# Kernel optimization log

Hardware: AMD Instinct MI355X
Metric: run time of the kernel (lower is better)

Reference implementation:

```python
import jax, jax.numpy as jnp
import numpy as np

NUM_HEADS = 8
WINDOW = 128  # num_previous_frames
EPS = 1e-5


def setup_inputs() -> dict:
    key = jax.random.key(0)
    ks = jax.random.split(key, 5)
    B, T, E = 8, 1024, 512
    x = jax.random.normal(ks[0], (B, T, E), dtype=jnp.float32)
    x_lengths = jax.random.randint(ks[1], (B,), 1, T + 1).astype(jnp.int32)
    gamma = jnp.ones((E,), dtype=jnp.float32)
    beta = jnp.zeros((E,), dtype=jnp.float32)
    sc_in = 1.0 / np.sqrt(E)
    w_in = jax.random.normal(ks[2], (3 * E, E), dtype=jnp.float32) * sc_in
    b_in = jnp.zeros((3 * E,), dtype=jnp.float32)
    w_out = jax.random.normal(ks[3], (E, E), dtype=jnp.float32) * sc_in
    b_out = jnp.zeros((E,), dtype=jnp.float32)
    return {"x": x, "x_lengths": x_lengths, "gamma": gamma, "beta": beta,
            "w_in": w_in, "b_in": b_in, "w_out": w_out, "b_out": b_out}


def _forward(x, gamma, beta, w_in, b_in, w_out, b_out):
    B, T, E = x.shape
    H = NUM_HEADS
    D = E // H
    # Timewise LayerNorm: normalize over channel dim per (batch, time)
    mu = jnp.mean(x, axis=-1, keepdims=True)
    var = jnp.mean(jnp.square(x - mu), axis=-1, keepdims=True)
    xn = (x - mu) * jax.lax.rsqrt(var + EPS) * gamma + beta
    # in-projection: qkv packed
    qkv = xn @ w_in.T + b_in  # [B,T,3E]
    q, k, v = jnp.split(qkv, 3, axis=-1)
    q = q.reshape(B, T, H, D)
    k = k.reshape(B, T, H, D)
    v = v.reshape(B, T, H, D)
    scale = 1.0 / np.sqrt(D)
    scores = jnp.einsum('bqhd,bkhd->bhqk', q * scale, k)  # [B,H,T,T]
    # banded causal mask: allow j in [i-WINDOW, i]
    i = jnp.arange(T)[:, None]
    j = jnp.arange(T)[None, :]
    allowed = (j <= i) & (j >= i - WINDOW)
    scores = jnp.where(allowed[None, None], scores, -jnp.inf)
    attn = jax.nn.softmax(scores, axis=-1)
    ctx = jnp.einsum('bhqk,bkhd->bqhd', attn, v).reshape(B, T, E)
    out = ctx @ w_out.T + b_out
    return out  # dropout is identity in eval mode


def reference(x, x_lengths, gamma, beta, w_in, b_in, w_out, b_out):
    del x_lengths  # unused by the original forward (no key_padding_mask passed)
    return _forward(x, gamma, beta, w_in, b_in, w_out, b_out)
```

## Files before the change

kernel.cpp:

```cpp
#include <hip/hip_runtime.h>
#include <stdint.h>

typedef __bf16 bf16;
typedef __bf16 bf16x8 __attribute__((ext_vector_type(8)));
typedef float f32x4 __attribute__((ext_vector_type(4)));

#define MFMA_16x16x32(a, b, c) __builtin_amdgcn_mfma_f32_16x16x32_bf16((a), (b), (c), 0, 0, 0)

__device__ __forceinline__ void gl_lds16(const bf16* g, bf16* l) {
    __builtin_amdgcn_global_load_lds(
        (const __attribute__((address_space(1))) void*)g,
        (__attribute__((address_space(3))) void*)l, 16, 0, 0);
}

__device__ __forceinline__ void prep_unit(int u, const float* __restrict__ x,
                                          const float* __restrict__ gamma,
                                          const float* __restrict__ beta,
                                          const float* __restrict__ w_in,
                                          const float* __restrict__ w_out,
                                          bf16* __restrict__ xn,
                                          bf16* __restrict__ cw_in,
                                          bf16* __restrict__ cw_out) {
    const int tid = threadIdx.x;
    if (u < 2048) {
        const int lane = tid & 63;
        const int row = (u << 2) + (tid >> 6);
        const size_t base = (size_t)row * 512 + lane * 8;
        const float* xf = x + base;
        float4 a = *(const float4*)xf;
        float4 b = *(const float4*)(xf + 4);
        float f[8] = {a.x, a.y, a.z, a.w, b.x, b.y, b.z, b.w};
        float s = 0.f;
#pragma unroll
        for (int j = 0; j < 8; ++j) s += f[j];
#pragma unroll
        for (int off = 32; off >= 1; off >>= 1) s += __shfl_xor(s, off, 64);
        const float mu = s * (1.0f / 512.0f);
        float vs = 0.f;
#pragma unroll
        for (int j = 0; j < 8; ++j) { float d = f[j] - mu; vs += d * d; }
#pragma unroll
        for (int off = 32; off >= 1; off >>= 1) vs += __shfl_xor(vs, off, 64);
        const float rstd = rsqrtf(vs * (1.0f / 512.0f) + 1e-5f);
        float4 g0 = *(const float4*)(gamma + lane * 8);
        float4 g1 = *(const float4*)(gamma + lane * 8 + 4);
        float4 b0 = *(const float4*)(beta + lane * 8);
        float4 b1 = *(const float4*)(beta + lane * 8 + 4);
        float gg[8] = {g0.x, g0.y, g0.z, g0.w, g1.x, g1.y, g1.z, g1.w};
        float bb[8] = {b0.x, b0.y, b0.z, b0.w, b1.x, b1.y, b1.z, b1.w};
        bf16x8 o;
#pragma unroll
        for (int j = 0; j < 8; ++j)
            o[j] = (bf16)((f[j] - mu) * rstd * gg[j] + bb[j]);
        *(bf16x8*)(xn + base) = o;
    } else {
        const float* src;
        bf16* dst;
        int base;
        if (u < 2432) { src = w_in;  dst = cw_in;  base = (u - 2048) * 2048; }
        else          { src = w_out; dst = cw_out; base = (u - 2432) * 2048; }
        const int i = base + tid * 8;
        float4 a = *(const float4*)(src + i);
        float4 b = *(const float4*)(src + i + 4);
        float f[8] = {a.x, a.y, a.z, a.w, b.x, b.y, b.z, b.w};
        bf16x8 o;
#pragma unroll
        for (int j = 0; j < 8; ++j) o[j] = (bf16)f[j];
        *(bf16x8*)(dst + i) = o;
    }
}

template <int TM, int TN, typename OT>
__device__ __forceinline__ void gemm_tile(const bf16* __restrict__ A,
                                          const bf16* __restrict__ B,
                                          const float* __restrict__ bias,
                                          OT* __restrict__ C,
                                          int N, int K, int m0, int n0,
                                          char* smem) {
    constexpr int MI = TM / 32, NI = TN / 32;
    bf16* As = (bf16*)smem;
    bf16* Bs = (bf16*)(smem + TM * 128);
    const int tid = threadIdx.x;
    const int lane = tid & 63;
    const int wid = tid >> 6;
    const int wm = (wid >> 1) * (TM / 2), wn = (wid & 1) * (TN / 2);
    const int l15 = lane & 15, l16 = lane >> 4;

    f32x4 acc[MI][NI] = {};

    const bf16* Abase = A + (size_t)m0 * K;
    const bf16* Bbase = B + (size_t)n0 * K;

    for (int k0 = 0; k0 < K; k0 += 64) {
#pragma unroll
        for (int c = tid; c < TM * 8; c += 256) {
            const int p = c / (TM * 4);
            const int r = (c % (TM * 4)) >> 2;
            const int ko = (c & 3) * 8 + p * 32;
            gl_lds16(Abase + (size_t)r * K + k0 + ko, &As[c * 8]);
        }
#pragma unroll
        for (int c = tid; c < TN * 8; c += 256) {
            const int p = c / (TN * 4);
            const int r = (c % (TN * 4)) >> 2;
            const int ko = (c & 3) * 8 + p * 32;
            gl_lds16(Bbase + (size_t)r * K + k0 + ko, &Bs[c * 8]);
        }
        __syncthreads();
#pragma unroll
        for (int h = 0; h < 2; ++h) {
            bf16x8 af[MI], bfr[NI];
#pragma unroll
            for (int t = 0; t < MI; ++t)
                af[t] = *(const bf16x8*)&As[h * (TM * 32) + (wm + t * 16 + l15) * 32 + l16 * 8];
#pragma unroll
            for (int t = 0; t < NI; ++t)
                bfr[t] = *(const bf16x8*)&Bs[h * (TN * 32) + (wn + t * 16 + l15) * 32 + l16 * 8];
#pragma unroll
            for (int i = 0; i < MI; ++i)
#pragma unroll
                for (int j = 0; j < NI; ++j)
                    acc[i][j] = MFMA_16x16x32(af[i], bfr[j], acc[i][j]);
        }
        __syncthreads();
    }

#pragma unroll
    for (int j = 0; j < NI; ++j) {
        const int col = n0 + wn + j * 16 + l15;
        const float bv = bias[col];
#pragma unroll
        for (int i = 0; i < MI; ++i) {
            const int rbase = m0 + wm + i * 16 + l16 * 4;
#pragma unroll
            for (int r = 0; r < 4; ++r)
                C[(size_t)(rbase + r) * N + col] = (OT)(acc[i][j][r] + bv);
        }
    }
}

#define KS_STRIDE 72
#define VN_STRIDE 74
#define PW_STRIDE 40

__device__ __forceinline__ void attn_unit(int qtile, int bh,
                                          const bf16* __restrict__ qkv,
                                          bf16* __restrict__ ctx,
                                          char* smem) {
    bf16* Ks   = (bf16*)smem;
    bf16* Vn   = (bf16*)(smem + 9216);
    bf16* Pbuf = (bf16*)(smem + 18688);

    const int tid = threadIdx.x;
    const int lane = tid & 63, wid = tid >> 6;
    const int l15 = lane & 15, l16 = lane >> 4;
    const int b = bh >> 3, h = bh & 7;
    const int q0 = qtile * 64;
    const int kv0 = (q0 > 128) ? (q0 - 128) : 0;
    const size_t tokbase = (size_t)b * 1024;

    const int qt0 = q0 + wid * 16;
    const bf16* qptr = qkv + (tokbase + qt0 + l15) * 1536 + h * 64;
    bf16x8 qa0 = *(const bf16x8*)(qptr + l16 * 8);
    bf16x8 qa1 = *(const bf16x8*)(qptr + 32 + l16 * 8);

    bf16* Pw = &Pbuf[wid * 16 * PW_STRIDE];
    f32x4 of[4] = {};
    float mst[4], lst[4];
#pragma unroll
    for (int r = 0; r < 4; ++r) { mst[r] = -1e30f; lst[r] = 0.f; }

    const int ktstart = ((qt0 > 128) ? (qt0 - 128) : 0) & ~31;
    const int ktend = qt0 + 15;

    for (int c0 = kv0; c0 < q0 + 64; c0 += 64) {
        for (int c = tid; c < 512; c += 256) {
            const int kk = c >> 3, dc = (c & 7) * 8;
            const bf16* src = qkv + (tokbase + c0 + kk) * 1536 + h * 64 + dc;
            *(uint4*)&Ks[kk * KS_STRIDE + dc] = *(const uint4*)(src + 512);
            uint4 vw = *(const uint4*)(src + 1024);
            uint* vdst = (uint*)&Vn[kk * VN_STRIDE + dc];
            vdst[0] = vw.x; vdst[1] = vw.y; vdst[2] = vw.z; vdst[3] = vw.w;
        }
        __syncthreads();

        const int klo = (ktstart > c0) ? ktstart : c0;
        const int khi = (ktend < c0 + 63) ? ktend : c0 + 63;
        for (int kt = klo; kt <= khi; kt += 32) {
            const int krel = kt - c0;
            f32x4 s0 = {}, s1 = {};
            {
                const bf16* kb0 = &Ks[(krel + l15) * KS_STRIDE + l16 * 8];
                const bf16* kb1 = kb0 + 16 * KS_STRIDE;
                s0 = MFMA_16x16x32(qa0, *(const bf16x8*)kb0, s0);
                s0 = MFMA_16x16x32(qa1, *(const bf16x8*)(kb0 + 32), s0);
                s1 = MFMA_16x16x32(qa0, *(const bf16x8*)kb1, s1);
                s1 = MFMA_16x16x32(qa1, *(const bf16x8*)(kb1 + 32), s1);
            }
            float e0[4], e1[4];
#pragma unroll
            for (int r = 0; r < 4; ++r) {
                const int qa = qt0 + l16 * 4 + r;
                const int kg0 = kt + l15;
                const int kg1 = kg0 + 16;
                const bool ok0 = (kg0 <= qa) && (kg0 >= qa - 128);
                const bool ok1 = (kg1 <= qa) && (kg1 >= qa - 128);
                float v0 = ok0 ? s0[r] * 0.125f : -1e30f;
                float v1 = ok1 ? s1[r] * 0.125f : -1e30f;
                float mx = fmaxf(v0, v1);
#pragma unroll
                for (int off = 1; off < 16; off <<= 1)
                    mx = fmaxf(mx, __shfl_xor(mx, off, 64));
                const float mnew = fmaxf(mst[r], mx);
                const float alpha = __expf(mst[r] - mnew);
                e0[r] = ok0 ? __expf(v0 - mnew) : 0.f;
                e1[r] = ok1 ? __expf(v1 - mnew) : 0.f;
                float rs = e0[r] + e1[r];
#pragma unroll
                for (int off = 1; off < 16; off <<= 1)
                    rs += __shfl_xor(rs, off, 64);
                lst[r] = lst[r] * alpha + rs;
                mst[r] = mnew;
#pragma unroll
                for (int nt = 0; nt < 4; ++nt) of[nt][r] *= alpha;
            }
#pragma unroll
            for (int r = 0; r < 4; ++r) {
                const int q = l16 * 4 + r;
                Pw[q * PW_STRIDE + l15] = (bf16)e0[r];
                Pw[q * PW_STRIDE + 16 + l15] = (bf16)e1[r];
            }
            __asm__ volatile("s_waitcnt lgkmcnt(0)" ::: "memory");
            bf16x8 pa = *(const bf16x8*)&Pw[l15 * PW_STRIDE + l16 * 8];
#pragma unroll
            for (int nt = 0; nt < 4; ++nt) {
                bf16x8 vb;
#pragma unroll
                for (int j = 0; j < 8; ++j)
                    vb[j] = Vn[(krel + l16 * 8 + j) * VN_STRIDE + nt * 16 + l15];
                of[nt] = MFMA_16x16x32(pa, vb, of[nt]);
            }
            __asm__ volatile("s_waitcnt lgkmcnt(0)" ::: "memory");
        }
        __syncthreads();
    }

    float linv[4];
#pragma unroll
    for (int r = 0; r < 4; ++r) linv[r] = 1.0f / lst[r];
    bf16* cbase = ctx + (tokbase + qt0) * 512 + h * 64;
#pragma unroll
    for (int nt = 0; nt < 4; ++nt)
#pragma unroll
        for (int r = 0; r < 4; ++r) {
            const int q = l16 * 4 + r;
            cbase[(size_t)q * 512 + nt * 16 + l15] = (bf16)(of[nt][r] * linv[r]);
        }
}

__global__ __launch_bounds__(256) void prep_kernel(const float* x, const float* gamma,
                                                   const float* beta, const float* w_in,
                                                   const float* w_out, bf16* xn,
                                                   bf16* cw_in, bf16* cw_out) {
    prep_unit(blockIdx.x, x, gamma, beta, w_in, w_out, xn, cw_in, cw_out);
}

__global__ __launch_bounds__(256) void gemm_qkv_kernel(const bf16* A, const bf16* B,
                                                       const float* bias, bf16* C) {
    __shared__ __align__(16) char smem[32768];
    gemm_tile<128, 128, bf16>(A, B, bias, C, 1536, 512,
                              blockIdx.y * 128, blockIdx.x * 128, smem);
}

__global__ __launch_bounds__(256) void attn_kernel(const bf16* qkv, bf16* ctx) {
    __shared__ __align__(16) char smem[23808];
    attn_unit(blockIdx.x >> 6, blockIdx.x & 63, qkv, ctx, smem);
}

__global__ __launch_bounds__(256) void gemm_out_kernel(const bf16* A, const bf16* B,
                                                       const float* bias, float* C) {
    __shared__ __align__(16) char smem[24576];
    gemm_tile<128, 64, float>(A, B, bias, C, 512, 512,
                              (blockIdx.x >> 3) * 128, (blockIdx.x & 7) * 64, smem);
}

extern "C" void kernel_launch(void* const* d_in, const int* in_sizes, int n_in,
                              void* d_out, int out_size, void* d_ws, size_t ws_size,
                              hipStream_t stream) {
    const float* x     = (const float*)d_in[0];
    const float* gamma = (const float*)d_in[2];
    const float* beta  = (const float*)d_in[3];
    const float* w_in  = (const float*)d_in[4];
    const float* b_in  = (const float*)d_in[5];
    const float* w_out = (const float*)d_in[6];
    const float* b_out = (const float*)d_in[7];
    float* out = (float*)d_out;
    char* ws = (char*)d_ws;

    bf16* cw_in  = (bf16*)ws;
    bf16* cw_out = cw_in + 786432;
    bf16* xn     = (bf16*)(ws + (4u << 20));
    bf16* qkv    = (bf16*)(ws + (12u << 20));
    bf16* ctx    = xn;

    prep_kernel<<<2560, 256, 0, stream>>>(x, gamma, beta, w_in, w_out, xn, cw_in, cw_out);
    gemm_qkv_kernel<<<dim3(12, 64), 256, 0, stream>>>(xn, cw_in, b_in, qkv);
    attn_kernel<<<1024, 256, 0, stream>>>(qkv, ctx);
    gemm_out_kernel<<<512, 256, 0, stream>>>(ctx, cw_out, b_out, out);
}
```

Baseline: 147.4 us.

## Load full KV window once in attention and retile both GEMMs

The attention kernel now loads the whole K/V window (up to 192 rows) into shared memory in one pass with a single barrier, replacing the chunked 64-row loop that had two barriers per chunk. V row indices are clamped to stay inside the loaded window. The QKV GEMM moves from 128x128 to 128x192 tiles (512 blocks), and the output GEMM moves from 128x64 to 64x128 tiles. The larger LDS footprint may lower attention occupancy, and the new GEMM tile shapes may not suit the generic tile template.

```diff
diff --git a/kernel.cpp b/kernel.cpp
--- a/kernel.cpp
+++ b/kernel.cpp
@@ -143,27 +143,37 @@
 #define VN_STRIDE 74
 #define PW_STRIDE 40
 
-__device__ __forceinline__ void attn_unit(int qtile, int bh,
-                                          const bf16* __restrict__ qkv,
-                                          bf16* __restrict__ ctx,
-                                          char* smem) {
-    bf16* Ks   = (bf16*)smem;
-    bf16* Vn   = (bf16*)(smem + 9216);
-    bf16* Pbuf = (bf16*)(smem + 18688);
+__global__ __launch_bounds__(256) void attn_kernel(const bf16* __restrict__ qkv,
+                                                   bf16* __restrict__ ctx) {
+    __shared__ alignas(16) bf16 Ks[192 * KS_STRIDE];
+    __shared__ alignas(16) bf16 Vn[192 * VN_STRIDE];
+    __shared__ alignas(16) bf16 Pbuf[4 * 16 * PW_STRIDE];
 
     const int tid = threadIdx.x;
     const int lane = tid & 63, wid = tid >> 6;
     const int l15 = lane & 15, l16 = lane >> 4;
-    const int b = bh >> 3, h = bh & 7;
-    const int q0 = qtile * 64;
+    const int bh = blockIdx.y, b = bh >> 3, h = bh & 7;
+    const int q0 = blockIdx.x * 64;
     const int kv0 = (q0 > 128) ? (q0 - 128) : 0;
+    const int nk = q0 + 64 - kv0;
     const size_t tokbase = (size_t)b * 1024;
+
+    for (int c = tid; c < nk * 8; c += 256) {
+        const int kk = c >> 3, dc = (c & 7) * 8;
+        const bf16* src = qkv + (tokbase + kv0 + kk) * 1536 + h * 64 + dc;
+        *(uint4*)&Ks[kk * KS_STRIDE + dc] = *(const uint4*)(src + 512);
+        uint4 vw = *(const uint4*)(src + 1024);
+        uint* vdst = (uint*)&Vn[kk * VN_STRIDE + dc];
+        vdst[0] = vw.x; vdst[1] = vw.y; vdst[2] = vw.z; vdst[3] = vw.w;
+    }
 
     const int qt0 = q0 + wid * 16;
     const bf16* qptr = qkv + (tokbase + qt0 + l15) * 1536 + h * 64;
     bf16x8 qa0 = *(const bf16x8*)(qptr + l16 * 8);
     bf16x8 qa1 = *(const bf16x8*)(qptr + 32 + l16 * 8);
 
+    __syncthreads();
+
     bf16* Pw = &Pbuf[wid * 16 * PW_STRIDE];
     f32x4 of[4] = {};
     float mst[4], lst[4];
@@ -171,78 +181,67 @@
     for (int r = 0; r < 4; ++r) { mst[r] = -1e30f; lst[r] = 0.f; }
 
     const int ktstart = ((qt0 > 128) ? (qt0 - 128) : 0) & ~31;
-    const int ktend = qt0 + 15;
-
-    for (int c0 = kv0; c0 < q0 + 64; c0 += 64) {
-        for (int c = tid; c < 512; c += 256) {
-            const int kk = c >> 3, dc = (c & 7) * 8;
-            const bf16* src = qkv + (tokbase + c0 + kk) * 1536 + h * 64 + dc;
-            *(uint4*)&Ks[kk * KS_STRIDE + dc] = *(const uint4*)(src + 512);
-            uint4 vw = *(const uint4*)(src + 1024);
-            uint* vdst = (uint*)&Vn[kk * VN_STRIDE + dc];
-            vdst[0] = vw.x; vdst[1] = vw.y; vdst[2] = vw.z; vdst[3] = vw.w;
-        }
-        __syncthreads();
-
-        const int klo = (ktstart > c0) ? ktstart : c0;
-        const int khi = (ktend < c0 + 63) ? ktend : c0 + 63;
-        for (int kt = klo; kt <= khi; kt += 32) {
-            const int krel = kt - c0;
-            f32x4 s0 = {}, s1 = {};
-            {
-                const bf16* kb0 = &Ks[(krel + l15) * KS_STRIDE + l16 * 8];
-                const bf16* kb1 = kb0 + 16 * KS_STRIDE;
-                s0 = MFMA_16x16x32(qa0, *(const bf16x8*)kb0, s0);
-                s0 = MFMA_16x16x32(qa1, *(const bf16x8*)(kb0 + 32), s0);
-                s1 = MFMA_16x16x32(qa0, *(const bf16x8*)kb1, s1);
-                s1 = MFMA_16x16x32(qa1, *(const bf16x8*)(kb1 + 32), s1);
-            }
-            float e0[4], e1[4];
-#pragma unroll
-            for (int r = 0; r < 4; ++r) {
-                const int qa = qt0 + l16 * 4 + r;
-                const int kg0 = kt + l15;
-                const int kg1 = kg0 + 16;
-                const bool ok0 = (kg0 <= qa) && (kg0 >= qa - 128);
-                const bool ok1 = (kg1 <= qa) && (kg1 >= qa - 128);
-                float v0 = ok0 ? s0[r] * 0.125f : -1e30f;
-                float v1 = ok1 ? s1[r] * 0.125f : -1e30f;
-                float mx = fmaxf(v0, v1);
-#pragma unroll
-                for (int off = 1; off < 16; off <<= 1)
-                    mx = fmaxf(mx, __shfl_xor(mx, off, 64));
-                const float mnew = fmaxf(mst[r], mx);
-                const float alpha = __expf(mst[r] - mnew);
-                e0[r] = ok0 ? __expf(v0 - mnew) : 0.f;
-                e1[r] = ok1 ? __expf(v1 - mnew) : 0.f;
-                float rs = e0[r] + e1[r];
-#pragma unroll
-                for (int off = 1; off < 16; off <<= 1)
-                    rs += __shfl_xor(rs, off, 64);
-                lst[r] = lst[r] * alpha + rs;
-                mst[r] = mnew;
-#pragma unroll
-                for (int nt = 0; nt < 4; ++nt) of[nt][r] *= alpha;
-            }
-#pragma unroll
-            for (int r = 0; r < 4; ++r) {
-                const int q = l16 * 4 + r;
-                Pw[q * PW_STRIDE + l15] = (bf16)e0[r];
-                Pw[q * PW_STRIDE + 16 + l15] = (bf16)e1[r];
-            }
-            __asm__ volatile("s_waitcnt lgkmcnt(0)" ::: "memory");
-            bf16x8 pa = *(const bf16x8*)&Pw[l15 * PW_STRIDE + l16 * 8];
-#pragma unroll
-            for (int nt = 0; nt < 4; ++nt) {
-                bf16x8 vb;
-#pragma unroll
-                for (int j = 0; j < 8; ++j)
-                    vb[j] = Vn[(krel + l16 * 8 + j) * VN_STRIDE + nt * 16 + l15];
-                of[nt] = MFMA_16x16x32(pa, vb, of[nt]);
-            }
-            __asm__ volatile("s_waitcnt lgkmcnt(0)" ::: "memory");
-        }
-        __syncthreads();
+    for (int kt = ktstart; kt <= qt0 + 15; kt += 32) {
+        const int krel = kt - kv0;
+        f32x4 s0 = {}, s1 = {};
+        {
+            const bf16* kb0 = &Ks[(krel + l15) * KS_STRIDE + l16 * 8];
+            const bf16* kb1 = kb0 + 16 * KS_STRIDE;
+            s0 = MFMA_16x16x32(qa0, *(const bf16x8*)kb0, s0);
+            s0 = MFMA_16x16x32(qa1, *(const bf16x8*)(kb0 + 32), s0);
+            s1 = MFMA_16x16x32(qa0, *(const bf16x8*)kb1, s1);
+            s1 = MFMA_16x16x32(qa1, *(const bf16x8*)(kb1 + 32), s1);
+        }
+        float e0[4], e1[4];
+#pragma unroll
+        for (int r = 0; r < 4; ++r) {
+            const int qa = qt0 + l16 * 4 + r;
+            const int kg0 = kt + l15;
+            const int kg1 = kg0 + 16;
+            const bool ok0 = (kg0 <= qa) && (kg0 >= qa - 128);
+            const bool ok1 = (kg1 <= qa) && (kg1 >= qa - 128);
+            float v0 = ok0 ? s0[r] * 0.125f : -1e30f;
+            float v1 = ok1 ? s1[r] * 0.125f : -1e30f;
+            float mx = fmaxf(v0, v1);
+#pragma unroll
+            for (int off = 1; off < 16; off <<= 1)
+                mx = fmaxf(mx, __shfl_xor(mx, off, 64));
+            const float mnew = fmaxf(mst[r], mx);
+            const float alpha = __expf(mst[r] - mnew);
+            e0[r] = ok0 ? __expf(v0 - mnew) : 0.f;
+            e1[r] = ok1 ? __expf(v1 - mnew) : 0.f;
+            float rs = e0[r] + e1[r];
+#pragma unroll
+            for (int off = 1; off < 16; off <<= 1)
+                rs += __shfl_xor(rs, off, 64);
+            lst[r] = lst[r] * alpha + rs;
+            mst[r] = mnew;
+#pragma unroll
+            for (int nt = 0; nt < 4; ++nt) of[nt][r] *= alpha;
+        }
+#pragma unroll
+        for (int r = 0; r < 4; ++r) {
+            const int q = l16 * 4 + r;
+            Pw[q * PW_STRIDE + l15] = (bf16)e0[r];
+            Pw[q * PW_STRIDE + 16 + l15] = (bf16)e1[r];
+        }
+        __asm__ volatile("s_waitcnt lgkmcnt(0)" ::: "memory");
+        bf16x8 pa = *(const bf16x8*)&Pw[l15 * PW_STRIDE + l16 * 8];
+        int row[8];
+#pragma unroll
+        for (int j = 0; j < 8; ++j) {
+            int rr = krel + l16 * 8 + j;
+            row[j] = (rr < nk) ? rr : (nk - 1);
+        }
+#pragma unroll
+        for (int nt = 0; nt < 4; ++nt) {
+            bf16x8 vb;
+#pragma unroll
+            for (int j = 0; j < 8; ++j)
+                vb[j] = Vn[row[j] * VN_STRIDE + nt * 16 + l15];
+            of[nt] = MFMA_16x16x32(pa, vb, of[nt]);
+        }
+        __asm__ volatile("s_waitcnt lgkmcnt(0)" ::: "memory");
     }
 
     float linv[4];
@@ -267,21 +266,16 @@
 
 __global__ __launch_bounds__(256) void gemm_qkv_kernel(const bf16* A, const bf16* B,
                                                        const float* bias, bf16* C) {
-    __shared__ __align__(16) char smem[32768];
-    gemm_tile<128, 128, bf16>(A, B, bias, C, 1536, 512,
-                              blockIdx.y * 128, blockIdx.x * 128, smem);
-}
-
-__global__ __launch_bounds__(256) void attn_kernel(const bf16* qkv, bf16* ctx) {
-    __shared__ __align__(16) char smem[23808];
-    attn_unit(blockIdx.x >> 6, blockIdx.x & 63, qkv, ctx, smem);
+    __shared__ __align__(16) char smem[40960];
+    gemm_tile<128, 192, bf16>(A, B, bias, C, 1536, 512,
+                              (blockIdx.x >> 3) * 128, (blockIdx.x & 7) * 192, smem);
 }
 
 __global__ __launch_bounds__(256) void gemm_out_kernel(const bf16* A, const bf16* B,
                                                        const float* bias, float* C) {
     __shared__ __align__(16) char smem[24576];
-    gemm_tile<128, 64, float>(A, B, bias, C, 512, 512,
-                              (blockIdx.x >> 3) * 128, (blockIdx.x & 7) * 64, smem);
+    gemm_tile<64, 128, float>(A, B, bias, C, 512, 512,
+                              (blockIdx.x >> 2) * 64, (blockIdx.x & 3) * 128, smem);
 }
 
 extern "C" void kernel_launch(void* const* d_in, const int* in_sizes, int n_in,
@@ -304,7 +298,7 @@
     bf16* ctx    = xn;
 
     prep_kernel<<<2560, 256, 0, stream>>>(x, gamma, beta, w_in, w_out, xn, cw_in, cw_out);
-    gemm_qkv_kernel<<<dim3(12, 64), 256, 0, stream>>>(xn, cw_in, b_in, qkv);
-    attn_kernel<<<1024, 256, 0, stream>>>(qkv, ctx);
+    gemm_qkv_kernel<<<512, 256, 0, stream>>>(xn, cw_in, b_in, qkv);
+    attn_kernel<<<dim3(16, 64), 256, 0, stream>>>(qkv, ctx);
     gemm_out_kernel<<<512, 256, 0, stream>>>(ctx, cw_out, b_out, out);
 }
```

Measured after the change: 154.1 us. 1.05x slower.
